# Optimization experiments

Measured on AMD Instinct MI355X. Metric: run time of the kernel, lower is better.

The kernel has to match this reference:

```python
import jax, jax.numpy as jnp
import numpy as np

B = 4194304
RAD2DEG = 180.0 / np.pi


def setup_inputs() -> dict:
    key = jax.random.key(0)
    k1, k2, k3 = jax.random.split(key, 3)
    label = jax.random.normal(k1, (B, 3, 2), dtype=jnp.float32)
    est_label = jax.random.normal(k2, (B, 6), dtype=jnp.float32)
    mix_way = jax.random.randint(k3, (B,), 0, 2, dtype=jnp.int32)  # 0='single', 1=mixed
    return {"label": label, "est_label": est_label, "mix_way": mix_way}


def reference(label, est_label, mix_way):
    # --- permutation-invariant MSE loss ---
    e1, e2 = est_label[:, :3], est_label[:, 3:]            # [B,3] each
    l1, l2 = label[:, :, 0], label[:, :, 1]                 # [B,3] each
    mse = lambda a, b: jnp.mean((a - b) ** 2, axis=-1)      # per-batch mean over 3 comps
    loss_perm1 = mse(e1, l1) + mse(e2, l2)                  # [B]
    loss_perm2 = mse(e2, l1) + mse(e1, l2)                  # [B]
    mixed_loss = jnp.minimum(loss_perm1, loss_perm2)        # [B]
    # 'single' branch in the original uses the FULL (unindexed) tensors -> same scalar each time
    single_loss = jnp.mean((est_label[:, :3] - label[:, :, 0]) ** 2)
    per_batch = jnp.where(mix_way == 0, single_loss, mixed_loss)
    label_loss = jnp.mean(per_batch)

    # --- azimuth MAE with angle wrap-around and best pairing ---
    lab_az1 = jnp.arctan2(label[:, 1, 0], label[:, 0, 0]) * RAD2DEG
    lab_az2 = jnp.arctan2(label[:, 1, 1], label[:, 0, 1]) * RAD2DEG
    est_az1 = jnp.arctan2(est_label[:, 1], est_label[:, 0]) * RAD2DEG
    est_az2 = jnp.arctan2(est_label[:, 4], est_label[:, 3]) * RAD2DEG

    def wrap(e):
        e = jnp.abs(e)
        return jnp.where(e > 180.0, 360.0 - e, e)

    e11 = wrap(lab_az1 - est_az1)
    e22 = wrap(lab_az2 - est_az2)
    e12 = wrap(lab_az1 - est_az2)
    e21 = wrap(lab_az2 - est_az1)

    use_direct = (e11 + e22) < (e12 + e21)
    mae1 = jnp.mean(jnp.where(use_direct, e11, e12))
    mae2 = jnp.mean(jnp.where(use_direct, e22, e21))

    return (label_loss, mae1, mae2)
```

## Files before the change

### kernel.cpp

```cpp
#include <hip/hip_runtime.h>
#include <math.h>

#define RAD2DEG 57.29577951308232f

constexpr int S1_BLOCKS = 2048;
constexpr int S1_TPB    = 256;
constexpr int NPAIR     = 4;

__device__ __forceinline__ float angdist_deg(float ax, float ay,
                                             float bx, float by) {
    float dot = ax * bx + ay * by;
    float cr  = fabsf(ay * bx - ax * by);
    float ad  = fabsf(dot);
    float mn  = fminf(cr, ad);
    float mx  = fmaxf(cr, ad);
    float t   = mn * __builtin_amdgcn_rcpf(fmaxf(mx, 1e-37f));
    float s   = t * t;
    float p = fmaf(s, -0.01172120f, 0.05265332f);
    p = fmaf(s, p, -0.11643287f);
    p = fmaf(s, p,  0.19354346f);
    p = fmaf(s, p, -0.33262347f);
    p = fmaf(s, p,  0.99997726f);
    float a = t * p;
    a = (cr > ad)    ? (1.57079632679489662f - a) : a;
    a = (dot < 0.0f) ? (3.14159265358979323f - a) : a;
    return a * RAD2DEG;
}

__device__ __forceinline__ void per_row(
    float l1x, float l2x, float l1y, float l2y, float l1z, float l2z,
    float e1x, float e1y, float e1z, float e2x, float e2y, float e2z,
    int mw,
    float& sS, float& sM, float& sC0, float& sM1, float& sM2)
{
    float dx, dy, dz;
    dx = e1x - l1x; dy = e1y - l1y; dz = e1z - l1z;
    float d11 = dx*dx + dy*dy + dz*dz;
    dx = e2x - l2x; dy = e2y - l2y; dz = e2z - l2z;
    float d22 = dx*dx + dy*dy + dz*dz;
    dx = e2x - l1x; dy = e2y - l1y; dz = e2z - l1z;
    float d21 = dx*dx + dy*dy + dz*dz;
    dx = e1x - l2x; dy = e1y - l2y; dz = e1z - l2z;
    float d12 = dx*dx + dy*dy + dz*dz;

    sS += d11;

    float mixed = fminf(d11 + d22, d21 + d12) * (1.0f / 3.0f);
    float m = (mw != 0) ? 1.0f : 0.0f;
    sM  += m * mixed;
    sC0 += 1.0f - m;

    float e11 = angdist_deg(l1x, l1y, e1x, e1y);
    float e22 = angdist_deg(l2x, l2y, e2x, e2y);
    float e12 = angdist_deg(l1x, l1y, e2x, e2y);
    float e21 = angdist_deg(l2x, l2y, e1x, e1y);

    bool ud = (e11 + e22) < (e12 + e21);
    sM1 += ud ? e11 : e12;
    sM2 += ud ? e22 : e21;
}

__device__ __forceinline__ void per_pair(
    const float4& L0, const float4& L1, const float4& L2,
    const float4& E0, const float4& E1, const float4& E2,
    const int2& mw,
    float& sS, float& sM, float& sC0, float& sM1, float& sM2)
{
    per_row(L0.x, L0.y, L0.z, L0.w, L1.x, L1.y,
            E0.x, E0.y, E0.z, E0.w, E1.x, E1.y,
            mw.x, sS, sM, sC0, sM1, sM2);
    per_row(L1.z, L1.w, L2.x, L2.y, L2.z, L2.w,
            E1.z, E1.w, E2.x, E2.y, E2.z, E2.w,
            mw.y, sS, sM, sC0, sM1, sM2);
}

__global__ __launch_bounds__(S1_TPB) void stage1_kernel(
    const float* __restrict__ label,
    const float* __restrict__ est,
    const int*   __restrict__ mix,
    float* __restrict__ partials,
    int P)
{
    const int tid   = threadIdx.x;
    const int wid   = tid >> 6;
    const int lane  = tid & 63;
    const int gsize = gridDim.x * S1_TPB;
    const int g     = blockIdx.x * S1_TPB + tid;

    const float4* lab4 = (const float4*)label;
    const float4* est4 = (const float4*)est;
    const int2*   mix2 = (const int2*)mix;

    float sS = 0.f, sM = 0.f, sC0 = 0.f, sM1 = 0.f, sM2 = 0.f;

    int p = g;
    for (; p + (NPAIR - 1) * gsize < P; p += NPAIR * gsize) {
        float4 Lv[NPAIR][3];
        float4 Ev[NPAIR][3];
        int2   Mv[NPAIR];
        #pragma unroll
        for (int k = 0; k < NPAIR; ++k) {
            const float4* lp = lab4 + (size_t)(p + k * gsize) * 3;
            Lv[k][0] = lp[0]; Lv[k][1] = lp[1]; Lv[k][2] = lp[2];
        }
        #pragma unroll
        for (int k = 0; k < NPAIR; ++k) {
            const float4* ep = est4 + (size_t)(p + k * gsize) * 3;
            Ev[k][0] = ep[0]; Ev[k][1] = ep[1]; Ev[k][2] = ep[2];
        }
        #pragma unroll
        for (int k = 0; k < NPAIR; ++k) {
            Mv[k] = mix2[p + k * gsize];
        }
        #pragma unroll
        for (int k = 0; k < NPAIR; ++k) {
            per_pair(Lv[k][0], Lv[k][1], Lv[k][2],
                     Ev[k][0], Ev[k][1], Ev[k][2],
                     Mv[k], sS, sM, sC0, sM1, sM2);
        }
    }
    for (; p < P; p += gsize) {
        const float4* lp = lab4 + (size_t)p * 3;
        const float4* ep = est4 + (size_t)p * 3;
        float4 L0 = lp[0], L1 = lp[1], L2 = lp[2];
        float4 E0 = ep[0], E1 = ep[1], E2 = ep[2];
        int2 mw = mix2[p];
        per_pair(L0, L1, L2, E0, E1, E2, mw, sS, sM, sC0, sM1, sM2);
    }

    for (int off = 32; off > 0; off >>= 1) {
        sS  += __shfl_down(sS,  off, 64);
        sM  += __shfl_down(sM,  off, 64);
        sC0 += __shfl_down(sC0, off, 64);
        sM1 += __shfl_down(sM1, off, 64);
        sM2 += __shfl_down(sM2, off, 64);
    }

    __shared__ float red[S1_TPB / 64][5];
    if (lane == 0) {
        red[wid][0] = sS; red[wid][1] = sM; red[wid][2] = sC0;
        red[wid][3] = sM1; red[wid][4] = sM2;
    }
    __syncthreads();
    if (tid == 0) {
        float r0 = 0.f, r1 = 0.f, r2 = 0.f, r3 = 0.f, r4 = 0.f;
        #pragma unroll
        for (int w = 0; w < S1_TPB / 64; ++w) {
            r0 += red[w][0]; r1 += red[w][1]; r2 += red[w][2];
            r3 += red[w][3]; r4 += red[w][4];
        }
        float* out = partials + (size_t)blockIdx.x * 5;
        out[0] = r0; out[1] = r1; out[2] = r2; out[3] = r3; out[4] = r4;
    }
}

__global__ __launch_bounds__(256) void stage2_kernel(
    const float* __restrict__ partials,
    float* __restrict__ out,
    int nblocks,
    long long Btot)
{
    const int tid = threadIdx.x;
    double aS = 0, aM = 0, aC0 = 0, aM1 = 0, aM2 = 0;
    for (int r = tid; r < nblocks; r += 256) {
        const float* row = partials + (size_t)r * 5;
        aS += row[0]; aM += row[1]; aC0 += row[2]; aM1 += row[3]; aM2 += row[4];
    }
    for (int off = 32; off > 0; off >>= 1) {
        aS  += __shfl_down(aS,  off, 64);
        aM  += __shfl_down(aM,  off, 64);
        aC0 += __shfl_down(aC0, off, 64);
        aM1 += __shfl_down(aM1, off, 64);
        aM2 += __shfl_down(aM2, off, 64);
    }
    __shared__ double red[4][5];
    const int wid = tid >> 6, lane = tid & 63;
    if (lane == 0) {
        red[wid][0] = aS; red[wid][1] = aM; red[wid][2] = aC0;
        red[wid][3] = aM1; red[wid][4] = aM2;
    }
    __syncthreads();
    if (tid == 0) {
        double S = 0, M = 0, C0 = 0, M1 = 0, M2 = 0;
        #pragma unroll
        for (int w = 0; w < 4; ++w) {
            S += red[w][0]; M += red[w][1]; C0 += red[w][2];
            M1 += red[w][3]; M2 += red[w][4];
        }
        const double Bd = (double)Btot;
        const double single_loss = S / (3.0 * Bd);
        out[0] = (float)((C0 * single_loss + M) / Bd);
        out[1] = (float)(M1 / Bd);
        out[2] = (float)(M2 / Bd);
    }
}

extern "C" void kernel_launch(void* const* d_in, const int* in_sizes, int n_in,
                              void* d_out, int out_size, void* d_ws, size_t ws_size,
                              hipStream_t stream) {
    const float* label = (const float*)d_in[0];
    const float* est   = (const float*)d_in[1];
    const int*   mix   = (const int*)d_in[2];
    float* out = (float*)d_out;
    float* partials = (float*)d_ws;

    const long long B = (long long)in_sizes[2];
    const int P = (int)(B / 2);

    stage1_kernel<<<S1_BLOCKS, S1_TPB, 0, stream>>>(label, est, mix, partials, P);
    stage2_kernel<<<1, 256, 0, stream>>>(partials, out, S1_BLOCKS, B);
}
```

Measured before the change: 231.8 us.

## Software-pipeline stage1 loads with double buffering and nontemporal loads, halve grid

After: 225.8 us, median of 2. -2.6%, faster.

```diff
diff --git a/kernel.cpp b/kernel.cpp
--- a/kernel.cpp
+++ b/kernel.cpp
@@ -3,9 +3,11 @@
 
 #define RAD2DEG 57.29577951308232f
 
-constexpr int S1_BLOCKS = 2048;
+constexpr int S1_BLOCKS = 1024;
 constexpr int S1_TPB    = 256;
-constexpr int NPAIR     = 4;
+
+typedef float f32x4 __attribute__((ext_vector_type(4)));
+typedef int   i32x2 __attribute__((ext_vector_type(2)));
 
 __device__ __forceinline__ float angdist_deg(float ax, float ay,
                                              float bx, float by) {
@@ -61,9 +63,9 @@
 }
 
 __device__ __forceinline__ void per_pair(
-    const float4& L0, const float4& L1, const float4& L2,
-    const float4& E0, const float4& E1, const float4& E2,
-    const int2& mw,
+    const f32x4& L0, const f32x4& L1, const f32x4& L2,
+    const f32x4& E0, const f32x4& E1, const f32x4& E2,
+    const i32x2& mw,
     float& sS, float& sM, float& sC0, float& sM1, float& sM2)
 {
     per_row(L0.x, L0.y, L0.z, L0.w, L1.x, L1.y,
@@ -87,46 +89,55 @@
     const int gsize = gridDim.x * S1_TPB;
     const int g     = blockIdx.x * S1_TPB + tid;
 
-    const float4* lab4 = (const float4*)label;
-    const float4* est4 = (const float4*)est;
-    const int2*   mix2 = (const int2*)mix;
+    const f32x4* lab4 = (const f32x4*)label;
+    const f32x4* est4 = (const f32x4*)est;
+    const i32x2* mix2 = (const i32x2*)mix;
 
     float sS = 0.f, sM = 0.f, sC0 = 0.f, sM1 = 0.f, sM2 = 0.f;
 
-    int p = g;
-    for (; p + (NPAIR - 1) * gsize < P; p += NPAIR * gsize) {
-        float4 Lv[NPAIR][3];
-        float4 Ev[NPAIR][3];
-        int2   Mv[NPAIR];
-        #pragma unroll
-        for (int k = 0; k < NPAIR; ++k) {
-            const float4* lp = lab4 + (size_t)(p + k * gsize) * 3;
-            Lv[k][0] = lp[0]; Lv[k][1] = lp[1]; Lv[k][2] = lp[2];
-        }
-        #pragma unroll
-        for (int k = 0; k < NPAIR; ++k) {
-            const float4* ep = est4 + (size_t)(p + k * gsize) * 3;
-            Ev[k][0] = ep[0]; Ev[k][1] = ep[1]; Ev[k][2] = ep[2];
-        }
-        #pragma unroll
-        for (int k = 0; k < NPAIR; ++k) {
-            Mv[k] = mix2[p + k * gsize];
-        }
-        #pragma unroll
-        for (int k = 0; k < NPAIR; ++k) {
-            per_pair(Lv[k][0], Lv[k][1], Lv[k][2],
-                     Ev[k][0], Ev[k][1], Ev[k][2],
-                     Mv[k], sS, sM, sC0, sM1, sM2);
-        }
-    }
-    for (; p < P; p += gsize) {
-        const float4* lp = lab4 + (size_t)p * 3;
-        const float4* ep = est4 + (size_t)p * 3;
-        float4 L0 = lp[0], L1 = lp[1], L2 = lp[2];
-        float4 E0 = ep[0], E1 = ep[1], E2 = ep[2];
-        int2 mw = mix2[p];
-        per_pair(L0, L1, L2, E0, E1, E2, mw, sS, sM, sC0, sM1, sM2);
-    }
+    f32x4 LA0, LA1, LA2, EA0, EA1, EA2; i32x2 MA;
+    f32x4 LB0, LB1, LB2, EB0, EB1, EB2; i32x2 MB;
+
+#define LOADP(L0, L1, L2, E0, E1, E2, M, idx) do {                     \
+        const f32x4* lp_ = lab4 + (size_t)(idx) * 3;                   \
+        const f32x4* ep_ = est4 + (size_t)(idx) * 3;                   \
+        L0 = __builtin_nontemporal_load(lp_ + 0);                      \
+        L1 = __builtin_nontemporal_load(lp_ + 1);                      \
+        L2 = __builtin_nontemporal_load(lp_ + 2);                      \
+        E0 = __builtin_nontemporal_load(ep_ + 0);                      \
+        E1 = __builtin_nontemporal_load(ep_ + 1);                      \
+        E2 = __builtin_nontemporal_load(ep_ + 2);                      \
+        M  = __builtin_nontemporal_load(mix2 + (idx));                 \
+    } while (0)
+
+    if (g < P) {
+        const int n = (P - 1 - g) / gsize + 1;
+        int pload = g + gsize;
+        LOADP(LA0, LA1, LA2, EA0, EA1, EA2, MA, g);
+        int nrem = n - 1;
+        while (nrem >= 2) {
+            LOADP(LB0, LB1, LB2, EB0, EB1, EB2, MB, pload);
+            pload += gsize;
+            per_pair(LA0, LA1, LA2, EA0, EA1, EA2, MA,
+                     sS, sM, sC0, sM1, sM2);
+            LOADP(LA0, LA1, LA2, EA0, EA1, EA2, MA, pload);
+            pload += gsize;
+            per_pair(LB0, LB1, LB2, EB0, EB1, EB2, MB,
+                     sS, sM, sC0, sM1, sM2);
+            nrem -= 2;
+        }
+        if (nrem == 1) {
+            LOADP(LB0, LB1, LB2, EB0, EB1, EB2, MB, pload);
+            per_pair(LA0, LA1, LA2, EA0, EA1, EA2, MA,
+                     sS, sM, sC0, sM1, sM2);
+            per_pair(LB0, LB1, LB2, EB0, EB1, EB2, MB,
+                     sS, sM, sC0, sM1, sM2);
+        } else {
+            per_pair(LA0, LA1, LA2, EA0, EA1, EA2, MA,
+                     sS, sM, sC0, sM1, sM2);
+        }
+    }
+#undef LOADP
 
     for (int off = 32; off > 0; off >>= 1) {
         sS  += __shfl_down(sS,  off, 64);
```
